# Kernel optimization log

Measured on AMD Instinct MI355X. Metric: run time of the kernel, lower is better.

The kernel has to match this reference:

```python
import jax, jax.numpy as jnp
import numpy as np

B, L, D, F = 4096, 200, 64, 100000


def setup_inputs() -> dict:
    key = jax.random.key(0)
    ks = jax.random.split(key, 12)
    film_hist = jax.random.randint(ks[0], (B, L), 0, F)                 # padded rated-film indices
    ratings = jax.random.uniform(ks[1], (B, L), jnp.float32) * 4.5 + 0.5  # letterboxd-style 0.5..5
    lengths = jax.random.randint(ks[2], (B,), 1, L + 1)                 # ragged history lengths (>=1)
    film_indices = jax.random.randint(ks[3], (B,), 0, F)                # target films to score
    emb_table = jax.random.normal(ks[4], (F, D), jnp.float32) * 0.1
    W1 = jax.random.normal(ks[5], (5 * D, 2 * D), jnp.float32) * 0.05
    b1 = jnp.zeros((2 * D,), jnp.float32)
    W2 = jax.random.normal(ks[6], (2 * D, D), jnp.float32) * 0.05
    b2 = jnp.zeros((D,), jnp.float32)
    W3 = jax.random.normal(ks[7], (D, 1), jnp.float32) * 0.05
    b3 = jnp.zeros((1,), jnp.float32)
    return {"film_hist": film_hist, "ratings": ratings, "lengths": lengths,
            "film_indices": film_indices, "emb_table": emb_table,
            "W1": W1, "b1": b1, "W2": W2, "b2": b2, "W3": W3, "b3": b3}


def _user_embeddings(film_hist, ratings, lengths, emb_table):
    # mask[b, l] = l < lengths[b]
    mask = jnp.arange(L)[None, :] < lengths[:, None]          # [B, L]
    n = lengths.astype(jnp.float32)                           # [B]
    mean_r = jnp.sum(jnp.where(mask, ratings, 0.0), axis=1) / n
    weights = ratings - mean_r[:, None] + 0.1                 # [B, L]
    hist_emb = emb_table[film_hist]                           # [B, L, D]
    w = hist_emb * weights[:, :, None]                        # weighted film embeddings
    m3 = mask[:, :, None]
    wmin = jnp.min(jnp.where(m3, w, jnp.inf), axis=1)
    wmax = jnp.max(jnp.where(m3, w, -jnp.inf), axis=1)
    wmean = jnp.sum(jnp.where(m3, w, 0.0), axis=1) / n[:, None]
    # median: sort valid entries (pads go to +inf at the end); torch.median
    # returns the lower middle element -> index (n-1)//2
    ws = jnp.sort(jnp.where(m3, w, jnp.inf), axis=1)
    mid = ((lengths - 1) // 2)[:, None, None]                 # [B,1,1]
    wmed = jnp.take_along_axis(ws, jnp.broadcast_to(mid, (B, 1, D)), axis=1)[:, 0, :]
    ue = jnp.concatenate([wmin, wmax, wmean, wmed], axis=1)   # [B, 4D]
    return ue / jnp.linalg.norm(ue, axis=1, keepdims=True)


def reference(film_hist, ratings, lengths, film_indices, emb_table, W1, b1, W2, b2, W3, b3):
    ue = _user_embeddings(film_hist, ratings, lengths, emb_table)  # [B, 4D]
    fe = emb_table[film_indices]                                   # [B, D]
    x = jnp.concatenate([ue, fe], axis=1)                          # [B, 5D]
    h = jax.nn.relu(x @ W1 + b1)   # Dropout(0.2) is identity in eval
    h = jax.nn.relu(h @ W2 + b2)
    return jax.nn.sigmoid(h @ W3 + b3)[:, 0]                       # [B]
```

## Files before the change

kernel.cpp:

```cpp
#include <hip/hip_runtime.h>
#include <hip/hip_bf16.h>
#include <stdint.h>


#define B_ 4096
#define L_ 200
#define D_ 64
#define LPAD 224
#define KP_U16 228

__global__ __launch_bounds__(512) void fused_kernel(
    const int* __restrict__ film_hist,
    const float* __restrict__ ratings,
    const int* __restrict__ lengths,
    const int* __restrict__ film_indices,
    const float* __restrict__ emb,
    const float* __restrict__ W1, const float* __restrict__ b1,
    const float* __restrict__ W2, const float* __restrict__ b2,
    const float* __restrict__ W3, const float* __restrict__ b3,
    float* __restrict__ out)
{
  __shared__ int   hist_s[LPAD];
  __shared__ float rat_s[LPAD];
  __shared__ float red[8];
  __shared__ float ue[4*D_];
  __shared__ float xls[320];
  __shared__ float red3[3*512];
  __shared__ union {
    uint16_t keys[D_*KP_U16];
    struct { float ph[512]; float h1s[128]; float h2s[64]; } m;
  } sh;

  const int b = blockIdx.x;
  const int t = threadIdx.x;
  const int w = t >> 6;
  const int lane = t & 63;
  const int n = lengths[b];
  const int cmax  = (n + 7) >> 3;
  const int cmax4 = (cmax + 3) & ~3;

  float r = 0.f;
  if (t < n) {
    hist_s[t] = film_hist[(size_t)b*L_ + t];
    float rv = ratings[(size_t)b*L_ + t];
    rat_s[t] = rv; r = rv;
  }
  if (t >= 448) {
    int fi = film_indices[b];
    xls[256 + (t-448)] = emb[(size_t)fi*D_ + (t-448)];
  }

  float s = r;
  #pragma unroll
  for (int off = 32; off; off >>= 1) s += __shfl_down(s, off);
  if (lane == 0) red[w] = s;
  __syncthreads();
  const float mean_r = (red[0]+red[1]+red[2]+red[3]+red[4]+red[5]+red[6]+red[7]) / (float)n;
  const float mr1 = 0.1f - mean_r;

  for (int l = n + t; l < 8*cmax4; l += 512) {
    hist_s[l] = hist_s[n-1];
    rat_s[l]  = rat_s[n-1];
  }
  __syncthreads();

  float vmin = __builtin_inff(), vmax = -__builtin_inff(), vsum = 0.f;
  uint16_t* kout = sh.keys + lane*KP_U16 + w*28;
  #pragma unroll
  for (int ch = 0; ch < 7; ++ch) {
    if (ch*4 < cmax4) {
      float vv[4], wg[4];
      int   ll[4];
      #pragma unroll
      for (int j = 0; j < 4; ++j) ll[j] = w + 8*(ch*4 + j);
      #pragma unroll
      for (int j = 0; j < 4; ++j) vv[j] = emb[(size_t)hist_s[ll[j]]*D_ + lane];
      #pragma unroll
      for (int j = 0; j < 4; ++j) wg[j] = rat_s[ll[j]] + mr1;
      uint32_t kk[4];
      #pragma unroll
      for (int j = 0; j < 4; ++j) {
        const float wv = vv[j] * wg[j];
        vmin = fminf(vmin, wv); vmax = fmaxf(vmax, wv);
        vsum += (ll[j] < n) ? wv : 0.f;
        uint32_t u = __float_as_uint(wv);
        kk[j] = (u ^ (0x80000000u | (uint32_t)((int32_t)u >> 31))) >> 16;
      }
      uint2 pr;
      pr.x = kk[0] | (kk[1] << 16);
      pr.y = kk[2] | (kk[3] << 16);
      *(uint2*)(kout + ch*4) = pr;
    }
  }
  red3[t] = vmin; red3[512 + t] = vmax; red3[1024 + t] = vsum;
  __syncthreads();

  if (t < 64) {
    float m = red3[t];
    #pragma unroll
    for (int ww = 1; ww < 8; ++ww) m = fminf(m, red3[ww*64 + t]);
    ue[t] = m;
  } else if (t < 128) {
    const int dd = t - 64;
    float m = red3[512 + dd];
    #pragma unroll
    for (int ww = 1; ww < 8; ++ww) m = fmaxf(m, red3[512 + ww*64 + dd]);
    ue[64 + dd] = m;
  } else if (t < 192) {
    const int dd = t - 128;
    float m = red3[1024 + dd];
    #pragma unroll
    for (int ww = 1; ww < 8; ++ww) m += red3[1024 + ww*64 + dd];
    ue[128 + dd] = m / (float)n;
  }

  const int sub  = lane >> 3;
  const int dsel = w*8 + (lane & 7);
  const uint16_t* kp = sh.keys + dsel*KP_U16 + sub*28;
  uint32_t W[16];
  #pragma unroll
  for (int i = 0; i < 7; ++i) {
    uint2 v = *(const uint2*)(kp + 4*i);
    W[2*i] = v.x; W[2*i+1] = v.y;
  }
  W[14] = 0u; W[15] = 0u;

  #define XS(k, jj, m) { uint32_t tt = ((W[k] ^ (W[(k)|(jj)] >> (jj))) & (m)); \
                         W[k] ^= tt; W[(k)|(jj)] ^= (tt << (jj)); }
  XS(0,8,0x00FF00FFu) XS(1,8,0x00FF00FFu) XS(2,8,0x00FF00FFu) XS(3,8,0x00FF00FFu)
  XS(4,8,0x00FF00FFu) XS(5,8,0x00FF00FFu) XS(6,8,0x00FF00FFu) XS(7,8,0x00FF00FFu)
  XS(0,4,0x0F0F0F0Fu) XS(1,4,0x0F0F0F0Fu) XS(2,4,0x0F0F0F0Fu) XS(3,4,0x0F0F0F0Fu)
  XS(8,4,0x0F0F0F0Fu) XS(9,4,0x0F0F0F0Fu) XS(10,4,0x0F0F0F0Fu) XS(11,4,0x0F0F0F0Fu)
  XS(0,2,0x33333333u) XS(1,2,0x33333333u) XS(4,2,0x33333333u) XS(5,2,0x33333333u)
  XS(8,2,0x33333333u) XS(9,2,0x33333333u) XS(12,2,0x33333333u) XS(13,2,0x33333333u)
  XS(0,1,0x55555555u) XS(2,1,0x55555555u) XS(4,1,0x55555555u) XS(6,1,0x55555555u)
  XS(8,1,0x55555555u) XS(10,1,0x55555555u) XS(12,1,0x55555555u) XS(14,1,0x55555555u)
  #undef XS

  const int c  = (n - sub + 7) >> 3;
  const int ce = (c + 1) >> 1, cf = c >> 1;
  uint32_t alive = ((1u << ce) - 1u) << (16 - ce);
  if (cf) alive |= ((1u << cf) - 1u) << (32 - cf);
  int k = (n - 1) >> 1;
  uint32_t prefix = 0;
  #pragma unroll
  for (int bb = 15; bb >= 0; --bb) {
    const uint32_t P = W[15 - bb];
    uint32_t z = alive & ~P;
    int cnt = __popc(z);
    cnt += __shfl_xor(cnt, 8);
    cnt += __shfl_xor(cnt, 16);
    cnt += __shfl_xor(cnt, 32);
    const bool zs = (k < cnt);
    alive  = zs ? z : (alive & P);
    k      = zs ? k : (k - cnt);
    prefix = zs ? prefix : (prefix | (1u << bb));
  }
  if (sub == 0) {
    uint32_t key32 = (prefix << 16) | 0x8000u;
    float med = (prefix & 0x8000u) ? __uint_as_float(key32 ^ 0x80000000u)
                                   : __uint_as_float(~key32);
    ue[192 + dsel] = med;
  }
  __syncthreads();

  float v = (t < 256) ? ue[t] : 0.f;
  float ss = v*v;
  #pragma unroll
  for (int off = 32; off; off >>= 1) ss += __shfl_down(ss, off);
  if (lane == 0) red[w] = ss;
  __syncthreads();
  const float rn2 = 1.0f / sqrtf(red[0]+red[1]+red[2]+red[3]+red[4]+red[5]+red[6]+red[7]);
  if (t < 256) xls[t] = v * rn2;
  __syncthreads();

  {
    const int j = t & 127, q = t >> 7;
    const float* Wp = W1 + (size_t)(q*80)*128 + j;
    const float* xp = xls + q*80;
    float a0 = 0.f, a1 = 0.f;
    #pragma unroll 8
    for (int i = 0; i < 80; i += 2) {
      a0 += xp[i]   * Wp[(size_t)i*128];
      a1 += xp[i+1] * Wp[(size_t)(i+1)*128];
    }
    sh.m.ph[t] = a0 + a1;
  }
  __syncthreads();
  if (t < 128) sh.m.h1s[t] = fmaxf(b1[t] + sh.m.ph[t] + sh.m.ph[t+128]
                                         + sh.m.ph[t+256] + sh.m.ph[t+384], 0.f);
  __syncthreads();

  {
    const int j = t & 63, q = t >> 6;
    const float* Wp = W2 + (size_t)(q*16)*64 + j;
    const float* hp = sh.m.h1s + q*16;
    float a = 0.f;
    #pragma unroll
    for (int i = 0; i < 16; ++i) a += hp[i] * Wp[(size_t)i*64];
    sh.m.ph[t] = a;
  }
  __syncthreads();
  if (t < 64) {
    float h = b2[t] + sh.m.ph[t] + sh.m.ph[t+64] + sh.m.ph[t+128] + sh.m.ph[t+192]
                    + sh.m.ph[t+256] + sh.m.ph[t+320] + sh.m.ph[t+384] + sh.m.ph[t+448];
    sh.m.h2s[t] = fmaxf(h, 0.f);
  }
  __syncthreads();

  if (t < 64) {
    float vv = sh.m.h2s[t] * W3[t];
    #pragma unroll
    for (int off = 32; off; off >>= 1) vv += __shfl_down(vv, off);
    if (t == 0) out[b] = 1.f / (1.f + __expf(-(vv + b3[0])));
  }
}

extern "C" void kernel_launch(void* const* d_in, const int* in_sizes, int n_in,
                              void* d_out, int out_size, void* d_ws, size_t ws_size,
                              hipStream_t stream) {
  const int*   film_hist = (const int*)d_in[0];
  const float* ratings   = (const float*)d_in[1];
  const int*   lengths   = (const int*)d_in[2];
  const int*   film_idx  = (const int*)d_in[3];
  const float* emb       = (const float*)d_in[4];
  const float* W1 = (const float*)d_in[5];
  const float* b1 = (const float*)d_in[6];
  const float* W2 = (const float*)d_in[7];
  const float* b2 = (const float*)d_in[8];
  const float* W3 = (const float*)d_in[9];
  const float* b3 = (const float*)d_in[10];

  fused_kernel<<<B_, 512, 0, stream>>>(film_hist, ratings, lengths, film_idx, emb,
                                       W1, b1, W2, b2, W3, b3, (float*)d_out);
}
```

Before: 61.69 us.

## Defer L2 normalization into layer-1 accumulation and use packed FMA in MLP

Layer 1 now runs on the unnormalized user embedding, with the norm reduction computed alongside it. The rescale is folded in afterwards as rn*sum_all + (1-rn)*film_part, which removes the sync-separated normalization pass. History padding now happens through clamped-index loads instead of a separate fill loop, dropping another barrier. Both MLP layers are reorganized to use v_pk_fma_f32 on float2 weight pairs with fewer partial-sum stages. The cost is extra accumulation work for the film-embedding rows and slightly different floating-point rounding.

Measured after the change: 82.06 us. 1.33x slower.

```diff
diff --git a/kernel.cpp b/kernel.cpp
--- a/kernel.cpp
+++ b/kernel.cpp
@@ -8,6 +8,14 @@
 #define D_ 64
 #define LPAD 224
 #define KP_U16 228
+
+typedef float v2f __attribute__((ext_vector_type(2)));
+
+__device__ __forceinline__ v2f pk_fma(v2f a, v2f b, v2f c) {
+  v2f d;
+  asm("v_pk_fma_f32 %0, %1, %2, %3" : "=v"(d) : "v"(a), "v"(b), "v"(c));
+  return d;
+}
 
 __global__ __launch_bounds__(512) void fused_kernel(
     const int* __restrict__ film_hist,
@@ -23,12 +31,11 @@
   __shared__ int   hist_s[LPAD];
   __shared__ float rat_s[LPAD];
   __shared__ float red[8];
-  __shared__ float ue[4*D_];
-  __shared__ float xls[320];
+  __shared__ float xraw[320];
   __shared__ float red3[3*512];
   __shared__ union {
     uint16_t keys[D_*KP_U16];
-    struct { float ph[512]; float h1s[128]; float h2s[64]; } m;
+    struct { v2f phA[512]; v2f phB[128]; float h1s[128]; } m;
   } sh;
 
   const int b = blockIdx.x;
@@ -40,14 +47,16 @@
   const int cmax4 = (cmax + 3) & ~3;
 
   float r = 0.f;
-  if (t < n) {
-    hist_s[t] = film_hist[(size_t)b*L_ + t];
-    float rv = ratings[(size_t)b*L_ + t];
-    rat_s[t] = rv; r = rv;
+  if (t < LPAD) {
+    const int idx = (t < n) ? t : (n - 1);
+    hist_s[t] = film_hist[(size_t)b*L_ + idx];
+    float rv = ratings[(size_t)b*L_ + idx];
+    rat_s[t] = rv;
+    r = (t < n) ? rv : 0.f;
   }
   if (t >= 448) {
     int fi = film_indices[b];
-    xls[256 + (t-448)] = emb[(size_t)fi*D_ + (t-448)];
+    xraw[256 + (t-448)] = emb[(size_t)fi*D_ + (t-448)];
   }
 
   float s = r;
@@ -57,12 +66,6 @@
   __syncthreads();
   const float mean_r = (red[0]+red[1]+red[2]+red[3]+red[4]+red[5]+red[6]+red[7]) / (float)n;
   const float mr1 = 0.1f - mean_r;
-
-  for (int l = n + t; l < 8*cmax4; l += 512) {
-    hist_s[l] = hist_s[n-1];
-    rat_s[l]  = rat_s[n-1];
-  }
-  __syncthreads();
 
   float vmin = __builtin_inff(), vmax = -__builtin_inff(), vsum = 0.f;
   uint16_t* kout = sh.keys + lane*KP_U16 + w*28;
@@ -99,19 +102,19 @@
     float m = red3[t];
     #pragma unroll
     for (int ww = 1; ww < 8; ++ww) m = fminf(m, red3[ww*64 + t]);
-    ue[t] = m;
+    xraw[t] = m;
   } else if (t < 128) {
     const int dd = t - 64;
     float m = red3[512 + dd];
     #pragma unroll
     for (int ww = 1; ww < 8; ++ww) m = fmaxf(m, red3[512 + ww*64 + dd]);
-    ue[64 + dd] = m;
+    xraw[64 + dd] = m;
   } else if (t < 192) {
     const int dd = t - 128;
     float m = red3[1024 + dd];
     #pragma unroll
     for (int ww = 1; ww < 8; ++ww) m += red3[1024 + ww*64 + dd];
-    ue[128 + dd] = m / (float)n;
+    xraw[128 + dd] = m / (float)n;
   }
 
   const int sub  = lane >> 3;
@@ -160,58 +163,95 @@
     uint32_t key32 = (prefix << 16) | 0x8000u;
     float med = (prefix & 0x8000u) ? __uint_as_float(key32 ^ 0x80000000u)
                                    : __uint_as_float(~key32);
-    ue[192 + dsel] = med;
-  }
-  __syncthreads();
-
-  float v = (t < 256) ? ue[t] : 0.f;
-  float ss = v*v;
-  #pragma unroll
-  for (int off = 32; off; off >>= 1) ss += __shfl_down(ss, off);
-  if (lane == 0) red[w] = ss;
-  __syncthreads();
-  const float rn2 = 1.0f / sqrtf(red[0]+red[1]+red[2]+red[3]+red[4]+red[5]+red[6]+red[7]);
-  if (t < 256) xls[t] = v * rn2;
+    xraw[192 + dsel] = med;
+  }
   __syncthreads();
 
   {
-    const int j = t & 127, q = t >> 7;
-    const float* Wp = W1 + (size_t)(q*80)*128 + j;
-    const float* xp = xls + q*80;
-    float a0 = 0.f, a1 = 0.f;
+    float v = (t < 256) ? xraw[t] : 0.f;
+    float ss = v*v;
+    #pragma unroll
+    for (int off = 32; off; off >>= 1) ss += __shfl_down(ss, off);
+    if (lane == 0) red[w] = ss;
+  }
+
+  {
+    const int jp = lane, q = w;
+    const float* Wp = W1 + 2*jp;
+    v2f accA = {0.f, 0.f};
     #pragma unroll 8
-    for (int i = 0; i < 80; i += 2) {
-      a0 += xp[i]   * Wp[(size_t)i*128];
-      a1 += xp[i+1] * Wp[(size_t)(i+1)*128];
-    }
-    sh.m.ph[t] = a0 + a1;
-  }
-  __syncthreads();
-  if (t < 128) sh.m.h1s[t] = fmaxf(b1[t] + sh.m.ph[t] + sh.m.ph[t+128]
-                                         + sh.m.ph[t+256] + sh.m.ph[t+384], 0.f);
+    for (int ii = 0; ii < 40; ++ii) {
+      const int i = q*40 + ii;
+      v2f wv = *(const v2f*)(Wp + (size_t)i*128);
+      const float xv = xraw[i];
+      v2f xx = {xv, xv};
+      accA = pk_fma(wv, xx, accA);
+    }
+    sh.m.phA[q*64 + jp] = accA;
+    if (q >= 6) {
+      v2f accB = {0.f, 0.f};
+      if (q == 6) {
+        #pragma unroll 8
+        for (int ii = 16; ii < 40; ++ii) {
+          const int i = 240 + ii;
+          v2f wv = *(const v2f*)(Wp + (size_t)i*128);
+          const float xv = xraw[i];
+          v2f xx = {xv, xv};
+          accB = pk_fma(wv, xx, accB);
+        }
+      } else {
+        #pragma unroll 8
+        for (int ii = 0; ii < 40; ++ii) {
+          const int i = 280 + ii;
+          v2f wv = *(const v2f*)(Wp + (size_t)i*128);
+          const float xv = xraw[i];
+          v2f xx = {xv, xv};
+          accB = pk_fma(wv, xx, accB);
+        }
+      }
+      sh.m.phB[(q-6)*64 + jp] = accB;
+    }
+  }
+  __syncthreads();
+
+  if (t < 64) {
+    const float rn = 1.0f / sqrtf(red[0]+red[1]+red[2]+red[3]+red[4]+red[5]+red[6]+red[7]);
+    v2f sA = sh.m.phA[t];
+    #pragma unroll
+    for (int q = 1; q < 8; ++q) sA += sh.m.phA[q*64 + t];
+    v2f sB = sh.m.phB[t] + sh.m.phB[64 + t];
+    float h0 = b1[2*t]   + rn*sA.x + (1.f-rn)*sB.x;
+    float h1 = b1[2*t+1] + rn*sA.y + (1.f-rn)*sB.y;
+    sh.m.h1s[2*t]   = fmaxf(h0, 0.f);
+    sh.m.h1s[2*t+1] = fmaxf(h1, 0.f);
+  }
   __syncthreads();
 
   {
-    const int j = t & 63, q = t >> 6;
-    const float* Wp = W2 + (size_t)(q*16)*64 + j;
-    const float* hp = sh.m.h1s + q*16;
-    float a = 0.f;
-    #pragma unroll
-    for (int i = 0; i < 16; ++i) a += hp[i] * Wp[(size_t)i*64];
-    sh.m.ph[t] = a;
-  }
-  __syncthreads();
-  if (t < 64) {
-    float h = b2[t] + sh.m.ph[t] + sh.m.ph[t+64] + sh.m.ph[t+128] + sh.m.ph[t+192]
-                    + sh.m.ph[t+256] + sh.m.ph[t+320] + sh.m.ph[t+384] + sh.m.ph[t+448];
-    sh.m.h2s[t] = fmaxf(h, 0.f);
-  }
-  __syncthreads();
-
-  if (t < 64) {
-    float vv = sh.m.h2s[t] * W3[t];
-    #pragma unroll
-    for (int off = 32; off; off >>= 1) vv += __shfl_down(vv, off);
+    const int jp2 = t & 31, q2 = t >> 5;
+    const float* Wp = W2 + 2*jp2;
+    v2f acc = {0.f, 0.f};
+    #pragma unroll
+    for (int ii = 0; ii < 8; ++ii) {
+      const int i = q2*8 + ii;
+      v2f wv = *(const v2f*)(Wp + (size_t)i*64);
+      const float xv = sh.m.h1s[i];
+      v2f xx = {xv, xv};
+      acc = pk_fma(wv, xx, acc);
+    }
+    sh.m.phA[q2*32 + jp2] = acc;
+  }
+  __syncthreads();
+
+  if (t < 32) {
+    v2f sA = sh.m.phA[t];
+    #pragma unroll
+    for (int q = 1; q < 16; ++q) sA += sh.m.phA[q*32 + t];
+    float g0 = fmaxf(b2[2*t]   + sA.x, 0.f);
+    float g1 = fmaxf(b2[2*t+1] + sA.y, 0.f);
+    float vv = g0*W3[2*t] + g1*W3[2*t+1];
+    #pragma unroll
+    for (int off = 16; off; off >>= 1) vv += __shfl_down(vv, off);
     if (t == 0) out[b] = 1.f / (1.f + __expf(-(vv + b3[0])));
   }
 }
```
